# Kernel tuning notes

Hardware: AMD Instinct MI355X
Metric: run time of the kernel (lower is better)

The kernel has to match this reference:

```python
import jax, jax.numpy as jnp
import numpy as np

N, D, HF, HS, E, TOPK = 4096, 1024, 2048, 4096, 8, 2
NUM_FRACTAL = 4  # int(8 * 0.5)
EPS_RMS = 1e-6


def setup_inputs() -> dict:
    key = jax.random.key(0)
    ks = jax.random.split(key, 9)
    s = 0.02
    return {
        "x": jax.random.normal(ks[0], (N, D), dtype=jnp.float32),
        "router_w": jax.random.normal(ks[1], (E, D), dtype=jnp.float32) * s,
        "frac_rms": jnp.ones((NUM_FRACTAL, D), jnp.float32),
        "frac_w1": jax.random.normal(ks[2], (NUM_FRACTAL, HF, D), dtype=jnp.float32) * s,
        "frac_w2": jax.random.normal(ks[3], (NUM_FRACTAL, D, HF), dtype=jnp.float32) * s,
        "frac_w3": jax.random.normal(ks[4], (NUM_FRACTAL, HF, D), dtype=jnp.float32) * s,
        "frac_gamma": jnp.full((NUM_FRACTAL, D), 1e-5, jnp.float32),
        "sw_w1": jax.random.normal(ks[5], (E - NUM_FRACTAL, HS, D), dtype=jnp.float32) * s,
        "sw_w2": jax.random.normal(ks[6], (E - NUM_FRACTAL, D, HS), dtype=jnp.float32) * s,
        "sw_w3": jax.random.normal(ks[7], (E - NUM_FRACTAL, HS, D), dtype=jnp.float32) * s,
    }


def _rmsnorm(x, w):
    return x * jax.lax.rsqrt(jnp.mean(x * x, axis=-1, keepdims=True) + EPS_RMS) * w


def _swiglu(x, w1, w2, w3):
    # torch Linear: y = x @ W.T
    return (jax.nn.silu(x @ w1.T) * (x @ w3.T)) @ w2.T


def _fractal(x, rms_w, w1, w2, w3, gamma):
    # depth=1 FractalBlock, eval mode (stochastic depth = identity)
    xn = _rmsnorm(x, rms_w)
    xn = xn + _swiglu(xn, w1, w2, w3)
    return gamma * xn + x


def _moe(x, router_w, frac_rms, frac_w1, frac_w2, frac_w3, frac_gamma,
         sw_w1, sw_w2, sw_w3):
    gate_logits = x @ router_w.T                      # [N, E]
    weights = jax.nn.softmax(gate_logits, axis=-1)
    top_w, top_i = jax.lax.top_k(weights, TOPK)        # [N, K]
    top_w = top_w / jnp.maximum(jnp.sum(top_w, axis=-1, keepdims=True), 1e-9)
    # dense combine weights: zero for unrouted experts (mathematically equal
    # to the gather/index_add dispatch in the original)
    combine = jnp.zeros((x.shape[0], E), x.dtype).at[
        jnp.arange(x.shape[0])[:, None], top_i].add(top_w)  # [N, E]

    out = jnp.zeros_like(x)
    for e in range(NUM_FRACTAL):
        out = out + combine[:, e:e + 1] * _fractal(
            x, frac_rms[e], frac_w1[e], frac_w2[e], frac_w3[e], frac_gamma[e])
    for j in range(E - NUM_FRACTAL):
        e = NUM_FRACTAL + j
        out = out + combine[:, e:e + 1] * _swiglu(x, sw_w1[j], sw_w2[j], sw_w3[j])
    return out


def reference(x, router_w, frac_rms, frac_w1, frac_w2, frac_w3, frac_gamma,
              sw_w1, sw_w2, sw_w3):
    return _moe(x, router_w, frac_rms, frac_w1, frac_w2, frac_w3, frac_gamma,
                sw_w1, sw_w2, sw_w3)
```

## Files before the change

kernel.cpp:

```cpp
#include <hip/hip_runtime.h>
#include <stdint.h>

#define N_TOK 4096
#define DIM   1024
#define HFRAC 2048
#define HSW   4096
#define NEXP  8
#define NFRAC 4
#define TOPK  2
#define TOTAL_ROWS (N_TOK * TOPK)
#define PAD_ROWS   (TOTAL_ROWS + 128)

typedef unsigned short u16;
typedef __bf16 bf16x8 __attribute__((ext_vector_type(8)));
typedef float  floatx4 __attribute__((ext_vector_type(4)));

struct alignas(8)  us4 { u16 v[4]; };
struct alignas(16) us8 { u16 v[8]; };

__device__ __forceinline__ u16 f32_to_bf16_raw(float f) {
    union { float f; uint32_t u; } v; v.f = f;
    uint32_t u = v.u;
    uint32_t r = 0x7FFFu + ((u >> 16) & 1u);
    return (u16)((u + r) >> 16);
}
__device__ __forceinline__ float bf16_raw_to_f32(u16 h) {
    union { uint32_t u; float f; } v; v.u = ((uint32_t)h) << 16;
    return v.f;
}

__device__ __forceinline__ int sw_addr(int row, int chunk) {
    return row * 64 + ((chunk ^ (row & 7)) << 3);
}

__global__ __launch_bounds__(256) void router_kernel(
    const float* __restrict__ x, const float* __restrict__ rw,
    int* __restrict__ re, float* __restrict__ rc, int* __restrict__ counts) {
    const int token = blockIdx.x * 4 + (threadIdx.x >> 6);
    const int lane  = threadIdx.x & 63;
    const float* xr = x + (size_t)token * DIM;

    float acc[NEXP];
#pragma unroll
    for (int e = 0; e < NEXP; ++e) acc[e] = 0.0f;
#pragma unroll
    for (int i = 0; i < DIM / 64; ++i) {
        int k = lane + i * 64;
        float xv = xr[k];
#pragma unroll
        for (int e = 0; e < NEXP; ++e) acc[e] += xv * rw[e * DIM + k];
    }
#pragma unroll
    for (int e = 0; e < NEXP; ++e) {
#pragma unroll
        for (int off = 32; off > 0; off >>= 1) acc[e] += __shfl_down(acc[e], off);
    }
    if (lane == 0) {
        float mx = acc[0];
#pragma unroll
        for (int e = 1; e < NEXP; ++e) mx = fmaxf(mx, acc[e]);
        float w[NEXP]; float s = 0.0f;
#pragma unroll
        for (int e = 0; e < NEXP; ++e) { w[e] = expf(acc[e] - mx); s += w[e]; }
        float inv = 1.0f / s;
#pragma unroll
        for (int e = 0; e < NEXP; ++e) w[e] *= inv;
        int i1 = 0;
#pragma unroll
        for (int e = 1; e < NEXP; ++e) if (w[e] > w[i1]) i1 = e;
        int i2 = (i1 == 0) ? 1 : 0;
#pragma unroll
        for (int e = 0; e < NEXP; ++e) if (e != i1 && w[e] > w[i2]) i2 = e;
        float denom = fmaxf(w[i1] + w[i2], 1e-9f);
        re[token]         = i1; rc[token]         = w[i1] / denom;
        re[N_TOK + token] = i2; rc[N_TOK + token] = w[i2] / denom;
        atomicAdd(&counts[i1], 1);
        atomicAdd(&counts[i2], 1);
    }
}

__global__ void offsets_kernel(const int* __restrict__ counts,
                               int* __restrict__ offs) {
    if (threadIdx.x == 0 && blockIdx.x == 0) {
        int a = 0;
#pragma unroll
        for (int e = 0; e < NEXP; ++e) { offs[e] = a; a += counts[e]; }
    }
}

__global__ __launch_bounds__(256) void scatter_kernel(
    const int* __restrict__ re, const float* __restrict__ rc,
    const int* __restrict__ offs, int* __restrict__ cursor,
    int* __restrict__ rowtok, float* __restrict__ co) {
    int token = blockIdx.x * 256 + threadIdx.x;
#pragma unroll
    for (int slot = 0; slot < TOPK; ++slot) {
        int e = re[slot * N_TOK + token];
        int i = atomicAdd(&cursor[e], 1);
        int r = offs[e] + i;
        rowtok[r] = token | (slot << 16);
        co[r]     = rc[slot * N_TOK + token];
    }
}

__global__ __launch_bounds__(256) void gather_norm_kernel(
    const float* __restrict__ x, const float* __restrict__ frac_rms,
    const int* __restrict__ rowtok, const int* __restrict__ offs,
    u16* __restrict__ Ag) {
    const int r   = blockIdx.x;
    const int tid = threadIdx.x;
    if (r >= TOTAL_ROWS) {
        us4 z = {0, 0, 0, 0};
        reinterpret_cast<us4*>(Ag + (size_t)r * DIM)[tid] = z;
        return;
    }
    int e = 0;
#pragma unroll
    for (int i = 1; i < NEXP; ++i) if (r >= offs[i]) e = i;
    const int token = rowtok[r] & 0xFFFF;
    float4 v = reinterpret_cast<const float4*>(x + (size_t)token * DIM)[tid];
    if (e < NFRAC) {
        float ss = v.x * v.x + v.y * v.y + v.z * v.z + v.w * v.w;
#pragma unroll
        for (int off = 32; off > 0; off >>= 1) ss += __shfl_down(ss, off);
        __shared__ float red[4];
        if ((tid & 63) == 0) red[tid >> 6] = ss;
        __syncthreads();
        float scale = rsqrtf((red[0] + red[1] + red[2] + red[3]) * (1.0f / DIM) + 1e-6f);
        float4 wv = reinterpret_cast<const float4*>(frac_rms + (size_t)e * DIM)[tid];
        v.x *= scale * wv.x; v.y *= scale * wv.y;
        v.z *= scale * wv.z; v.w *= scale * wv.w;
    }
    us4 o = { f32_to_bf16_raw(v.x), f32_to_bf16_raw(v.y),
              f32_to_bf16_raw(v.z), f32_to_bf16_raw(v.w) };
    reinterpret_cast<us4*>(Ag + (size_t)r * DIM)[tid] = o;
}

#define BM 128
#define BN 64
#define BK 64

__global__ __launch_bounds__(256) void gemm1_kernel(
    const u16* __restrict__ Ag,
    const float* __restrict__ frac_w1, const float* __restrict__ frac_w3,
    const float* __restrict__ sw_w1,   const float* __restrict__ sw_w3,
    u16* __restrict__ gbuf,
    const int* __restrict__ counts, const int* __restrict__ offs) {
    const int e   = blockIdx.z;
    const int cnt = counts[e];
    const int m0  = blockIdx.y * BM;
    if (m0 >= cnt) return;
    const int Ne = (e < NFRAC) ? HFRAC : HSW;
    const int n0 = blockIdx.x * BN;
    if (n0 >= Ne) return;
    const int rowbase = offs[e];
    const float* W1 = (e < NFRAC) ? frac_w1 + (size_t)e * HFRAC * DIM
                                  : sw_w1 + (size_t)(e - NFRAC) * HSW * DIM;
    const float* W3 = (e < NFRAC) ? frac_w3 + (size_t)e * HFRAC * DIM
                                  : sw_w3 + (size_t)(e - NFRAC) * HSW * DIM;
    const u16* A = Ag + (size_t)(rowbase + m0) * DIM;

    __shared__ u16 sA[BM * BK];
    __shared__ u16 sB1[BN * BK];
    __shared__ u16 sB3[BN * BK];

    const int tid  = threadIdx.x;
    const int wave = tid >> 6;
    const int lane = tid & 63;

    floatx4 acc1[2][4], acc3[2][4];
    floatx4 zero = { 0.f, 0.f, 0.f, 0.f };
#pragma unroll
    for (int mt = 0; mt < 2; ++mt)
#pragma unroll
        for (int nt = 0; nt < 4; ++nt) { acc1[mt][nt] = zero; acc3[mt][nt] = zero; }

    for (int k0 = 0; k0 < DIM; k0 += BK) {
#pragma unroll
        for (int it = 0; it < 4; ++it) {
            int idx = it * 2048 + tid * 8;
            int r = idx >> 6, c = idx & 63;
            int4 v = *reinterpret_cast<const int4*>(A + (size_t)r * DIM + k0 + c);
            *reinterpret_cast<int4*>(&sA[sw_addr(r, c >> 3)]) = v;
        }
#pragma unroll
        for (int it = 0; it < 2; ++it) {
            int idx = it * 2048 + tid * 8;
            int r = idx >> 6, c = idx & 63;
            size_t go = (size_t)(n0 + r) * DIM + k0 + c;
            float4 a1 = *reinterpret_cast<const float4*>(W1 + go);
            float4 b1 = *reinterpret_cast<const float4*>(W1 + go + 4);
            float4 a3 = *reinterpret_cast<const float4*>(W3 + go);
            float4 b3 = *reinterpret_cast<const float4*>(W3 + go + 4);
            us8 o1 = { f32_to_bf16_raw(a1.x), f32_to_bf16_raw(a1.y),
                       f32_to_bf16_raw(a1.z), f32_to_bf16_raw(a1.w),
                       f32_to_bf16_raw(b1.x), f32_to_bf16_raw(b1.y),
                       f32_to_bf16_raw(b1.z), f32_to_bf16_raw(b1.w) };
            us8 o3 = { f32_to_bf16_raw(a3.x), f32_to_bf16_raw(a3.y),
                       f32_to_bf16_raw(a3.z), f32_to_bf16_raw(a3.w),
                       f32_to_bf16_raw(b3.x), f32_to_bf16_raw(b3.y),
                       f32_to_bf16_raw(b3.z), f32_to_bf16_raw(b3.w) };
            *reinterpret_cast<us8*>(&sB1[sw_addr(r, c >> 3)]) = o1;
            *reinterpret_cast<us8*>(&sB3[sw_addr(r, c >> 3)]) = o3;
        }
        __syncthreads();
#pragma unroll
        for (int ks = 0; ks < 2; ++ks) {
            const int chunk = ks * 4 + (lane >> 4);
            bf16x8 af[2], b1f[4], b3f[4];
#pragma unroll
            for (int mt = 0; mt < 2; ++mt) {
                int ra = wave * 32 + mt * 16 + (lane & 15);
                af[mt] = *reinterpret_cast<const bf16x8*>(&sA[sw_addr(ra, chunk)]);
            }
#pragma unroll
            for (int nt = 0; nt < 4; ++nt) {
                int rb = nt * 16 + (lane & 15);
                b1f[nt] = *reinterpret_cast<const bf16x8*>(&sB1[sw_addr(rb, chunk)]);
                b3f[nt] = *reinterpret_cast<const bf16x8*>(&sB3[sw_addr(rb, chunk)]);
            }
#pragma unroll
            for (int mt = 0; mt < 2; ++mt)
#pragma unroll
                for (int nt = 0; nt < 4; ++nt) {
                    acc1[mt][nt] = __builtin_amdgcn_mfma_f32_16x16x32_bf16(
                        af[mt], b1f[nt], acc1[mt][nt], 0, 0, 0);
                    acc3[mt][nt] = __builtin_amdgcn_mfma_f32_16x16x32_bf16(
                        af[mt], b3f[nt], acc3[mt][nt], 0, 0, 0);
                }
        }
        __syncthreads();
    }
#pragma unroll
    for (int mt = 0; mt < 2; ++mt)
#pragma unroll
        for (int nt = 0; nt < 4; ++nt)
#pragma unroll
            for (int r = 0; r < 4; ++r) {
                int row_local = m0 + wave * 32 + mt * 16 + (lane >> 4) * 4 + r;
                if (row_local >= cnt) continue;
                int col = n0 + nt * 16 + (lane & 15);
                float h1 = acc1[mt][nt][r];
                float h3 = acc3[mt][nt][r];
                float g = (h1 / (1.0f + expf(-h1))) * h3;
                gbuf[(size_t)(rowbase + row_local) * HSW + col] = f32_to_bf16_raw(g);
            }
}

__global__ __launch_bounds__(256) void gemm2_kernel(
    const u16* __restrict__ gbuf,
    const float* __restrict__ frac_w2, const float* __restrict__ sw_w2,
    const u16* __restrict__ Ag, const float* __restrict__ x,
    const float* __restrict__ frac_gamma,
    const int* __restrict__ rowtok, const float* __restrict__ co,
    const int* __restrict__ counts, const int* __restrict__ offs,
    float* __restrict__ ybuf) {
    const int e   = blockIdx.z;
    const int cnt = counts[e];
    const int m0  = blockIdx.y * BM;
    if (m0 >= cnt) return;
    const int n0 = blockIdx.x * BN;
    const int Ke = (e < NFRAC) ? HFRAC : HSW;
    const int rowbase = offs[e];
    const float* W2 = (e < NFRAC) ? frac_w2 + (size_t)e * DIM * HFRAC
                                  : sw_w2 + (size_t)(e - NFRAC) * DIM * HSW;
    const u16* A = gbuf + (size_t)(rowbase + m0) * HSW;

    __shared__ u16 sA[BM * BK];
    __shared__ u16 sB[BN * BK];

    const int tid  = threadIdx.x;
    const int wave = tid >> 6;
    const int lane = tid & 63;

    floatx4 acc[2][4];
    floatx4 zero = { 0.f, 0.f, 0.f, 0.f };
#pragma unroll
    for (int mt = 0; mt < 2; ++mt)
#pragma unroll
        for (int nt = 0; nt < 4; ++nt) acc[mt][nt] = zero;

    for (int k0 = 0; k0 < Ke; k0 += BK) {
#pragma unroll
        for (int it = 0; it < 4; ++it) {
            int idx = it * 2048 + tid * 8;
            int r = idx >> 6, c = idx & 63;
            int4 v = *reinterpret_cast<const int4*>(A + (size_t)r * HSW + k0 + c);
            *reinterpret_cast<int4*>(&sA[sw_addr(r, c >> 3)]) = v;
        }
#pragma unroll
        for (int it = 0; it < 2; ++it) {
            int idx = it * 2048 + tid * 8;
            int r = idx >> 6, c = idx & 63;
            size_t go = (size_t)(n0 + r) * Ke + k0 + c;
            float4 a = *reinterpret_cast<const float4*>(W2 + go);
            float4 b = *reinterpret_cast<const float4*>(W2 + go + 4);
            us8 o = { f32_to_bf16_raw(a.x), f32_to_bf16_raw(a.y),
                      f32_to_bf16_raw(a.z), f32_to_bf16_raw(a.w),
                      f32_to_bf16_raw(b.x), f32_to_bf16_raw(b.y),
                      f32_to_bf16_raw(b.z), f32_to_bf16_raw(b.w) };
            *reinterpret_cast<us8*>(&sB[sw_addr(r, c >> 3)]) = o;
        }
        __syncthreads();
#pragma unroll
        for (int ks = 0; ks < 2; ++ks) {
            const int chunk = ks * 4 + (lane >> 4);
            bf16x8 af[2], bf[4];
#pragma unroll
            for (int mt = 0; mt < 2; ++mt) {
                int ra = wave * 32 + mt * 16 + (lane & 15);
                af[mt] = *reinterpret_cast<const bf16x8*>(&sA[sw_addr(ra, chunk)]);
            }
#pragma unroll
            for (int nt = 0; nt < 4; ++nt) {
                int rb = nt * 16 + (lane & 15);
                bf[nt] = *reinterpret_cast<const bf16x8*>(&sB[sw_addr(rb, chunk)]);
            }
#pragma unroll
            for (int mt = 0; mt < 2; ++mt)
#pragma unroll
                for (int nt = 0; nt < 4; ++nt)
                    acc[mt][nt] = __builtin_amdgcn_mfma_f32_16x16x32_bf16(
                        af[mt], bf[nt], acc[mt][nt], 0, 0, 0);
        }
        __syncthreads();
    }
    const float* gamma = frac_gamma + (size_t)e * DIM;
#pragma unroll
    for (int mt = 0; mt < 2; ++mt)
#pragma unroll
        for (int nt = 0; nt < 4; ++nt)
#pragma unroll
            for (int rr = 0; rr < 4; ++rr) {
                int row_local = m0 + wave * 32 + mt * 16 + (lane >> 4) * 4 + rr;
                if (row_local >= cnt) continue;
                int r = rowbase + row_local;
                int col = n0 + nt * 16 + (lane & 15);
                int info  = rowtok[r];
                int token = info & 0xFFFF;
                int slot  = info >> 16;
                float coef = co[r];
                float y = acc[mt][nt][rr];
                float val;
                if (e < NFRAC) {
                    float xn = bf16_raw_to_f32(Ag[(size_t)r * DIM + col]);
                    val = coef * (gamma[col] * (xn + y) + x[(size_t)token * DIM + col]);
                } else {
                    val = coef * y;
                }
                ybuf[(size_t)slot * N_TOK * DIM + (size_t)token * DIM + col] = val;
            }
}

__global__ __launch_bounds__(256) void combine_kernel(
    const float* __restrict__ ybuf, float* __restrict__ out) {
    size_t i = (size_t)blockIdx.x * 256 + threadIdx.x;
    float4 a = reinterpret_cast<const float4*>(ybuf)[i];
    float4 b = reinterpret_cast<const float4*>(ybuf + (size_t)N_TOK * DIM)[i];
    float4 o = { a.x + b.x, a.y + b.y, a.z + b.z, a.w + b.w };
    reinterpret_cast<float4*>(out)[i] = o;
}

extern "C" void kernel_launch(void* const* d_in, const int* in_sizes, int n_in,
                              void* d_out, int out_size, void* d_ws, size_t ws_size,
                              hipStream_t stream) {
    const float* x          = (const float*)d_in[0];
    const float* router_w   = (const float*)d_in[1];
    const float* frac_rms   = (const float*)d_in[2];
    const float* frac_w1    = (const float*)d_in[3];
    const float* frac_w2    = (const float*)d_in[4];
    const float* frac_w3    = (const float*)d_in[5];
    const float* frac_gamma = (const float*)d_in[6];
    const float* sw_w1      = (const float*)d_in[7];
    const float* sw_w2      = (const float*)d_in[8];
    const float* sw_w3      = (const float*)d_in[9];
    float* out = (float*)d_out;

    char* ws = (char*)d_ws;
    int*   counts = (int*)ws;
    int*   cursor = (int*)(ws + 32);
    int*   offs   = (int*)(ws + 64);
    int*   re     = (int*)(ws + 256);
    float* rc     = (float*)(ws + 256 + (32u << 10));
    int*   rowtok = (int*)(ws + 256 + (64u << 10));
    float* co     = (float*)(ws + 256 + (112u << 10));
    u16*   Ag     = (u16*)(ws + (1u << 18));
    u16*   gbuf   = (u16*)(ws + (size_t)18 * (1u << 20));
    float* ybuf   = (float*)(ws + (size_t)88 * (1u << 20));

    hipMemsetAsync(ws, 0, 256, stream);

    router_kernel<<<N_TOK / 4, 256, 0, stream>>>(x, router_w, re, rc, counts);
    offsets_kernel<<<1, 64, 0, stream>>>(counts, offs);
    scatter_kernel<<<N_TOK / 256, 256, 0, stream>>>(re, rc, offs, cursor, rowtok, co);
    gather_norm_kernel<<<PAD_ROWS, 256, 0, stream>>>(x, frac_rms, rowtok, offs, Ag);

    gemm1_kernel<<<dim3(HSW / BN, TOTAL_ROWS / BM, NEXP), 256, 0, stream>>>(
        Ag, frac_w1, frac_w3, sw_w1, sw_w3, gbuf, counts, offs);

    gemm2_kernel<<<dim3(DIM / BN, TOTAL_ROWS / BM, NEXP), 256, 0, stream>>>(
        gbuf, frac_w2, sw_w2, Ag, x, frac_gamma, rowtok, co, counts, offs, ybuf);

    combine_kernel<<<(N_TOK * DIM) / (4 * 256), 256, 0, stream>>>(ybuf, out);
}
```

Baseline: 834.8 us.

## Pre-convert expert weights to bf16 and use direct global-to-LDS loads with 128x128 tiles

Adds a conversion pass that turns the fp32 expert weights into bf16 buffers in workspace before each GEMM, so the GEMM kernels no longer convert weights per tile. Both GEMMs now load A and B tiles with global_load_lds directly into LDS, and the output tile grows from 128x64 to 128x128 with a 2x2 wave layout. This removes redundant per-block weight conversion and register staging and improves reuse of the A tile. In exchange it adds extra full passes over roughly 200MB of fp32 weights each call, drops the XOR swizzle (risking LDS bank conflicts), and reuses workspace regions between W1b/W2b and W3b/ybuf.

```diff
diff --git a/kernel.cpp b/kernel.cpp
--- a/kernel.cpp
+++ b/kernel.cpp
@@ -16,7 +16,6 @@
 typedef float  floatx4 __attribute__((ext_vector_type(4)));
 
 struct alignas(8)  us4 { u16 v[4]; };
-struct alignas(16) us8 { u16 v[8]; };
 
 __device__ __forceinline__ u16 f32_to_bf16_raw(float f) {
     union { float f; uint32_t u; } v; v.f = f;
@@ -29,8 +28,10 @@
     return v.f;
 }
 
-__device__ __forceinline__ int sw_addr(int row, int chunk) {
-    return row * 64 + ((chunk ^ (row & 7)) << 3);
+__device__ __forceinline__ void gload16(const void* g, void* l) {
+    __builtin_amdgcn_global_load_lds(
+        (const __attribute__((address_space(1))) void*)g,
+        (__attribute__((address_space(3))) void*)l, 16, 0, 0);
 }
 
 __global__ __launch_bounds__(256) void router_kernel(
@@ -136,15 +137,30 @@
     reinterpret_cast<us4*>(Ag + (size_t)r * DIM)[tid] = o;
 }
 
+#define FA4 (NFRAC * HFRAC * DIM / 4)
+#define SA4 ((NEXP - NFRAC) * HSW * DIM / 4)
+#define CVT_BLOCKS ((FA4 + SA4) / 256)
+
+__global__ __launch_bounds__(256) void cvt_pair_kernel(
+    const float* __restrict__ a, const float* __restrict__ b,
+    u16* __restrict__ dst) {
+    size_t i = (size_t)blockIdx.x * 256 + threadIdx.x;
+    const float4* src; size_t off;
+    if (i < (size_t)FA4) { src = (const float4*)a; off = i; }
+    else                 { src = (const float4*)b; off = i - FA4; }
+    float4 v = src[off];
+    us4 o = { f32_to_bf16_raw(v.x), f32_to_bf16_raw(v.y),
+              f32_to_bf16_raw(v.z), f32_to_bf16_raw(v.w) };
+    reinterpret_cast<us4*>(dst)[i] = o;
+}
+
 #define BM 128
-#define BN 64
+#define BN 128
 #define BK 64
 
 __global__ __launch_bounds__(256) void gemm1_kernel(
-    const u16* __restrict__ Ag,
-    const float* __restrict__ frac_w1, const float* __restrict__ frac_w3,
-    const float* __restrict__ sw_w1,   const float* __restrict__ sw_w3,
-    u16* __restrict__ gbuf,
+    const u16* __restrict__ Ag, const u16* __restrict__ W1b,
+    const u16* __restrict__ W3b, u16* __restrict__ gbuf,
     const int* __restrict__ counts, const int* __restrict__ offs) {
     const int e   = blockIdx.z;
     const int cnt = counts[e];
@@ -154,92 +170,71 @@
     const int n0 = blockIdx.x * BN;
     if (n0 >= Ne) return;
     const int rowbase = offs[e];
-    const float* W1 = (e < NFRAC) ? frac_w1 + (size_t)e * HFRAC * DIM
-                                  : sw_w1 + (size_t)(e - NFRAC) * HSW * DIM;
-    const float* W3 = (e < NFRAC) ? frac_w3 + (size_t)e * HFRAC * DIM
-                                  : sw_w3 + (size_t)(e - NFRAC) * HSW * DIM;
-    const u16* A = Ag + (size_t)(rowbase + m0) * DIM;
+    const size_t wofs = (e < NFRAC)
+        ? (size_t)e * HFRAC * DIM
+        : (size_t)NFRAC * HFRAC * DIM + (size_t)(e - NFRAC) * HSW * DIM;
+    const u16* W1 = W1b + wofs + (size_t)n0 * DIM;
+    const u16* W3 = W3b + wofs + (size_t)n0 * DIM;
+    const u16* A  = Ag + (size_t)(rowbase + m0) * DIM;
 
     __shared__ u16 sA[BM * BK];
     __shared__ u16 sB1[BN * BK];
     __shared__ u16 sB3[BN * BK];
 
     const int tid  = threadIdx.x;
+    const int lane = tid & 63;
     const int wave = tid >> 6;
-    const int lane = tid & 63;
-
-    floatx4 acc1[2][4], acc3[2][4];
+    const int wr   = wave >> 1, wc = wave & 1;
+    const int rlo  = lane & 15, khi = lane >> 4;
+
+    floatx4 acc1[4][4], acc3[4][4];
     floatx4 zero = { 0.f, 0.f, 0.f, 0.f };
 #pragma unroll
-    for (int mt = 0; mt < 2; ++mt)
+    for (int mt = 0; mt < 4; ++mt)
 #pragma unroll
         for (int nt = 0; nt < 4; ++nt) { acc1[mt][nt] = zero; acc3[mt][nt] = zero; }
 
     for (int k0 = 0; k0 < DIM; k0 += BK) {
 #pragma unroll
         for (int it = 0; it < 4; ++it) {
-            int idx = it * 2048 + tid * 8;
-            int r = idx >> 6, c = idx & 63;
-            int4 v = *reinterpret_cast<const int4*>(A + (size_t)r * DIM + k0 + c);
-            *reinterpret_cast<int4*>(&sA[sw_addr(r, c >> 3)]) = v;
+            int ci = it * 256 + tid;
+            int r = ci >> 3, c = (ci & 7) * 8;
+            gload16(A  + (size_t)r * DIM + k0 + c, &sA [ci * 8]);
+            gload16(W1 + (size_t)r * DIM + k0 + c, &sB1[ci * 8]);
+            gload16(W3 + (size_t)r * DIM + k0 + c, &sB3[ci * 8]);
         }
-#pragma unroll
-        for (int it = 0; it < 2; ++it) {
-            int idx = it * 2048 + tid * 8;
-            int r = idx >> 6, c = idx & 63;
-            size_t go = (size_t)(n0 + r) * DIM + k0 + c;
-            float4 a1 = *reinterpret_cast<const float4*>(W1 + go);
-            float4 b1 = *reinterpret_cast<const float4*>(W1 + go + 4);
-            float4 a3 = *reinterpret_cast<const float4*>(W3 + go);
-            float4 b3 = *reinterpret_cast<const float4*>(W3 + go + 4);
-            us8 o1 = { f32_to_bf16_raw(a1.x), f32_to_bf16_raw(a1.y),
-                       f32_to_bf16_raw(a1.z), f32_to_bf16_raw(a1.w),
-                       f32_to_bf16_raw(b1.x), f32_to_bf16_raw(b1.y),
-                       f32_to_bf16_raw(b1.z), f32_to_bf16_raw(b1.w) };
-            us8 o3 = { f32_to_bf16_raw(a3.x), f32_to_bf16_raw(a3.y),
-                       f32_to_bf16_raw(a3.z), f32_to_bf16_raw(a3.w),
-                       f32_to_bf16_raw(b3.x), f32_to_bf16_raw(b3.y),
-                       f32_to_bf16_raw(b3.z), f32_to_bf16_raw(b3.w) };
-            *reinterpret_cast<us8*>(&sB1[sw_addr(r, c >> 3)]) = o1;
-            *reinterpret_cast<us8*>(&sB3[sw_addr(r, c >> 3)]) = o3;
-        }
         __syncthreads();
 #pragma unroll
         for (int ks = 0; ks < 2; ++ks) {
-            const int chunk = ks * 4 + (lane >> 4);
-            bf16x8 af[2], b1f[4], b3f[4];
-#pragma unroll
-            for (int mt = 0; mt < 2; ++mt) {
-                int ra = wave * 32 + mt * 16 + (lane & 15);
-                af[mt] = *reinterpret_cast<const bf16x8*>(&sA[sw_addr(ra, chunk)]);
+            const int co = (ks * 4 + khi) * 8;
+            bf16x8 af[4], b1[4], b3[4];
+#pragma unroll
+            for (int t = 0; t < 4; ++t) {
+                af[t] = *reinterpret_cast<const bf16x8*>(&sA [(wr * 64 + t * 16 + rlo) * BK + co]);
+                b1[t] = *reinterpret_cast<const bf16x8*>(&sB1[(wc * 64 + t * 16 + rlo) * BK + co]);
+                b3[t] = *reinterpret_cast<const bf16x8*>(&sB3[(wc * 64 + t * 16 + rlo) * BK + co]);
             }
 #pragma unroll
-            for (int nt = 0; nt < 4; ++nt) {
-                int rb = nt * 16 + (lane & 15);
-                b1f[nt] = *reinterpret_cast<const bf16x8*>(&sB1[sw_addr(rb, chunk)]);
-                b3f[nt] = *reinterpret_cast<const bf16x8*>(&sB3[sw_addr(rb, chunk)]);
-            }
-#pragma unroll
-            for (int mt = 0; mt < 2; ++mt)
+            for (int mt = 0; mt < 4; ++mt)
 #pragma unroll
                 for (int nt = 0; nt < 4; ++nt) {
                     acc1[mt][nt] = __builtin_amdgcn_mfma_f32_16x16x32_bf16(
-                        af[mt], b1f[nt], acc1[mt][nt], 0, 0, 0);
+                        af[mt], b1[nt], acc1[mt][nt], 0, 0, 0);
                     acc3[mt][nt] = __builtin_amdgcn_mfma_f32_16x16x32_bf16(
-                        af[mt], b3f[nt], acc3[mt][nt], 0, 0, 0);
+                        af[mt], b3[nt], acc3[mt][nt], 0, 0, 0);
                 }
         }
         __syncthreads();
     }
 #pragma unroll
-    for (int mt = 0; mt < 2; ++mt)
+    for (int mt = 0; mt < 4; ++mt)
 #pragma unroll
         for (int nt = 0; nt < 4; ++nt)
 #pragma unroll
             for (int r = 0; r < 4; ++r) {
-                int row_local = m0 + wave * 32 + mt * 16 + (lane >> 4) * 4 + r;
+                int row_local = m0 + wr * 64 + mt * 16 + khi * 4 + r;
                 if (row_local >= cnt) continue;
-                int col = n0 + nt * 16 + (lane & 15);
+                int col = n0 + wc * 64 + nt * 16 + rlo;
                 float h1 = acc1[mt][nt][r];
                 float h3 = acc3[mt][nt][r];
                 float g = (h1 / (1.0f + expf(-h1))) * h3;
@@ -248,8 +243,7 @@
 }
 
 __global__ __launch_bounds__(256) void gemm2_kernel(
-    const u16* __restrict__ gbuf,
-    const float* __restrict__ frac_w2, const float* __restrict__ sw_w2,
+    const u16* __restrict__ gbuf, const u16* __restrict__ W2b,
     const u16* __restrict__ Ag, const float* __restrict__ x,
     const float* __restrict__ frac_gamma,
     const int* __restrict__ rowtok, const float* __restrict__ co,
@@ -262,62 +256,48 @@
     const int n0 = blockIdx.x * BN;
     const int Ke = (e < NFRAC) ? HFRAC : HSW;
     const int rowbase = offs[e];
-    const float* W2 = (e < NFRAC) ? frac_w2 + (size_t)e * DIM * HFRAC
-                                  : sw_w2 + (size_t)(e - NFRAC) * DIM * HSW;
-    const u16* A = gbuf + (size_t)(rowbase + m0) * HSW;
+    const size_t wofs = (e < NFRAC)
+        ? (size_t)e * DIM * HFRAC
+        : (size_t)NFRAC * DIM * HFRAC + (size_t)(e - NFRAC) * DIM * HSW;
+    const u16* W2 = W2b + wofs + (size_t)n0 * Ke;
+    const u16* A  = gbuf + (size_t)(rowbase + m0) * HSW;
 
     __shared__ u16 sA[BM * BK];
     __shared__ u16 sB[BN * BK];
 
     const int tid  = threadIdx.x;
+    const int lane = tid & 63;
     const int wave = tid >> 6;
-    const int lane = tid & 63;
-
-    floatx4 acc[2][4];
+    const int wr   = wave >> 1, wc = wave & 1;
+    const int rlo  = lane & 15, khi = lane >> 4;
+
+    floatx4 acc[4][4];
     floatx4 zero = { 0.f, 0.f, 0.f, 0.f };
 #pragma unroll
-    for (int mt = 0; mt < 2; ++mt)
+    for (int mt = 0; mt < 4; ++mt)
 #pragma unroll
         for (int nt = 0; nt < 4; ++nt) acc[mt][nt] = zero;
 
     for (int k0 = 0; k0 < Ke; k0 += BK) {
 #pragma unroll
         for (int it = 0; it < 4; ++it) {
-            int idx = it * 2048 + tid * 8;
-            int r = idx >> 6, c = idx & 63;
-            int4 v = *reinterpret_cast<const int4*>(A + (size_t)r * HSW + k0 + c);
-            *reinterpret_cast<int4*>(&sA[sw_addr(r, c >> 3)]) = v;
+            int ci = it * 256 + tid;
+            int r = ci >> 3, c = (ci & 7) * 8;
+            gload16(A  + (size_t)r * HSW + k0 + c, &sA[ci * 8]);
+            gload16(W2 + (size_t)r * Ke  + k0 + c, &sB[ci * 8]);
         }
-#pragma unroll
-        for (int it = 0; it < 2; ++it) {
-            int idx = it * 2048 + tid * 8;
-            int r = idx >> 6, c = idx & 63;
-            size_t go = (size_t)(n0 + r) * Ke + k0 + c;
-            float4 a = *reinterpret_cast<const float4*>(W2 + go);
-            float4 b = *reinterpret_cast<const float4*>(W2 + go + 4);
-            us8 o = { f32_to_bf16_raw(a.x), f32_to_bf16_raw(a.y),
-                      f32_to_bf16_raw(a.z), f32_to_bf16_raw(a.w),
-                      f32_to_bf16_raw(b.x), f32_to_bf16_raw(b.y),
-                      f32_to_bf16_raw(b.z), f32_to_bf16_raw(b.w) };
-            *reinterpret_cast<us8*>(&sB[sw_addr(r, c >> 3)]) = o;
-        }
         __syncthreads();
 #pragma unroll
         for (int ks = 0; ks < 2; ++ks) {
-            const int chunk = ks * 4 + (lane >> 4);
-            bf16x8 af[2], bf[4];
-#pragma unroll
-            for (int mt = 0; mt < 2; ++mt) {
-                int ra = wave * 32 + mt * 16 + (lane & 15);
-                af[mt] = *reinterpret_cast<const bf16x8*>(&sA[sw_addr(ra, chunk)]);
+            const int co = (ks * 4 + khi) * 8;
+            bf16x8 af[4], bf[4];
+#pragma unroll
+            for (int t = 0; t < 4; ++t) {
+                af[t] = *reinterpret_cast<const bf16x8*>(&sA[(wr * 64 + t * 16 + rlo) * BK + co]);
+                bf[t] = *reinterpret_cast<const bf16x8*>(&sB[(wc * 64 + t * 16 + rlo) * BK + co]);
             }
 #pragma unroll
-            for (int nt = 0; nt < 4; ++nt) {
-                int rb = nt * 16 + (lane & 15);
-                bf[nt] = *reinterpret_cast<const bf16x8*>(&sB[sw_addr(rb, chunk)]);
-            }
-#pragma unroll
-            for (int mt = 0; mt < 2; ++mt)
+            for (int mt = 0; mt < 4; ++mt)
 #pragma unroll
                 for (int nt = 0; nt < 4; ++nt)
                     acc[mt][nt] = __builtin_amdgcn_mfma_f32_16x16x32_bf16(
@@ -327,15 +307,15 @@
     }
     const float* gamma = frac_gamma + (size_t)e * DIM;
 #pragma unroll
-    for (int mt = 0; mt < 2; ++mt)
+    for (int mt = 0; mt < 4; ++mt)
 #pragma unroll
         for (int nt = 0; nt < 4; ++nt)
 #pragma unroll
             for (int rr = 0; rr < 4; ++rr) {
-                int row_local = m0 + wave * 32 + mt * 16 + (lane >> 4) * 4 + rr;
+                int row_local = m0 + wr * 64 + mt * 16 + khi * 4 + rr;
                 if (row_local >= cnt) continue;
                 int r = rowbase + row_local;
-                int col = n0 + nt * 16 + (lane & 15);
+                int col = n0 + wc * 64 + nt * 16 + rlo;
                 int info  = rowtok[r];
                 int token = info & 0xFFFF;
                 int slot  = info >> 16;
@@ -385,10 +365,16 @@
     int*   rowtok = (int*)(ws + 256 + (64u << 10));
     float* co     = (float*)(ws + 256 + (112u << 10));
     u16*   Ag     = (u16*)(ws + (1u << 18));
-    u16*   gbuf   = (u16*)(ws + (size_t)18 * (1u << 20));
-    float* ybuf   = (float*)(ws + (size_t)88 * (1u << 20));
+    u16*   gbuf   = (u16*)(ws + (size_t)18  * (1u << 20));
+    u16*   W1b    = (u16*)(ws + (size_t)84  * (1u << 20));
+    u16*   W3b    = (u16*)(ws + (size_t)132 * (1u << 20));
+    u16*   W2b    = (u16*)(ws + (size_t)84  * (1u << 20));
+    float* ybuf   = (float*)(ws + (size_t)132 * (1u << 20));
 
     hipMemsetAsync(ws, 0, 256, stream);
+
+    cvt_pair_kernel<<<CVT_BLOCKS, 256, 0, stream>>>(frac_w1, sw_w1, W1b);
+    cvt_pair_kernel<<<CVT_BLOCKS, 256, 0, stream>>>(frac_w3, sw_w3, W3b);
 
     router_kernel<<<N_TOK / 4, 256, 0, stream>>>(x, router_w, re, rc, counts);
     offsets_kernel<<<1, 64, 0, stream>>>(counts, offs);
@@ -396,10 +382,12 @@
     gather_norm_kernel<<<PAD_ROWS, 256, 0, stream>>>(x, frac_rms, rowtok, offs, Ag);
 
     gemm1_kernel<<<dim3(HSW / BN, TOTAL_ROWS / BM, NEXP), 256, 0, stream>>>(
-        Ag, frac_w1, frac_w3, sw_w1, sw_w3, gbuf, counts, offs);
+        Ag, W1b, W3b, gbuf, counts, offs);
+
+    cvt_pair_kernel<<<CVT_BLOCKS, 256, 0, stream>>>(frac_w2, sw_w2, W2b);
 
     gemm2_kernel<<<dim3(DIM / BN, TOTAL_ROWS / BM, NEXP), 256, 0, stream>>>(
-        gbuf, frac_w2, sw_w2, Ag, x, frac_gamma, rowtok, co, counts, offs, ybuf);
+        gbuf, W2b, Ag, x, frac_gamma, rowtok, co, counts, offs, ybuf);
 
     combine_kernel<<<(N_TOK * DIM) / (4 * 256), 256, 0, stream>>>(ybuf, out);
 }
```

Result: slower. 1.020 ms (+22.2%).
